# Performance work log

Measured on AMD Instinct MI355X. Metric: run time of the kernel, lower is better.

The kernel has to match this reference:

```python
import jax, jax.numpy as jnp
import numpy as np

D = 256
H = 256
B = 128
T = 512


def _init_cell(key, input_size, hidden_size):
    K = 1.0 / np.sqrt(hidden_size)
    k1, k2, k3, k4 = jax.random.split(key, 4)
    u = lambda k, shape: jax.random.uniform(k, shape, jnp.float32, -K, K)
    return (u(k1, (3 * hidden_size, input_size)),
            u(k2, (3 * hidden_size, hidden_size)),
            u(k3, (3 * hidden_size,)),
            u(k4, (3 * hidden_size,)))


def setup_inputs() -> dict:
    key = jax.random.key(0)
    kx, kf, kb = jax.random.split(key, 3)
    x = jax.random.normal(kx, (B, T, D), dtype=jnp.float32)
    w_ih_fw, w_hh_fw, b_ih_fw, b_hh_fw = _init_cell(kf, D, H)
    w_ih_bw, w_hh_bw, b_ih_bw, b_hh_bw = _init_cell(kb, D, H)
    return {
        "x": x,
        "w_ih_fw": w_ih_fw, "w_hh_fw": w_hh_fw, "b_ih_fw": b_ih_fw, "b_hh_fw": b_hh_fw,
        "w_ih_bw": w_ih_bw, "w_hh_bw": w_hh_bw, "b_ih_bw": b_ih_bw, "b_hh_bw": b_hh_bw,
    }


def _gru_scan(x_tbd, w_ih, w_hh, b_ih, b_hh):
    # x_tbd: [T, B, D]; returns outputs [T, B, H] and final h [B, H]
    h0 = jnp.zeros((x_tbd.shape[1], H), dtype=x_tbd.dtype)

    def step(h, x_t):
        xT = x_t @ w_ih.T + b_ih          # [B, 3H]
        hT = h @ w_hh.T + b_hh            # [B, 3H]
        s = jax.nn.sigmoid(xT + hT)
        r = s[:, :H]
        z = s[:, H:2 * H]
        n = jnp.tanh(xT[:, 2 * H:] + r * hT[:, 2 * H:])
        h_new = (1.0 - z) * n + z * h
        return h_new, h_new

    h_last, outs = jax.lax.scan(step, h0, x_tbd)
    return outs, h_last


def reference(x, w_ih_fw, w_hh_fw, b_ih_fw, b_hh_fw,
              w_ih_bw, w_hh_bw, b_ih_bw, b_hh_bw):
    x_tbd = jnp.swapaxes(x, 0, 1)                         # [T, B, D]
    outs_fw, h_fw = _gru_scan(x_tbd, w_ih_fw, w_hh_fw, b_ih_fw, b_hh_fw)
    outs_bw_rev, h_bw = _gru_scan(x_tbd[::-1], w_ih_bw, w_hh_bw, b_ih_bw, b_hh_bw)
    outs_bw = outs_bw_rev[::-1]
    outputs = jnp.concatenate([outs_fw, outs_bw], axis=-1)  # [T, B, 2H]
    outputs = jnp.swapaxes(outputs, 0, 1)                   # [B, T, 2H]
    return outputs, h_fw, h_bw
```

## Files before the change

### kernel.cpp

```cpp
#include <hip/hip_runtime.h>
#include <stdint.h>
#include <stddef.h>

#define T_ 512
#define B_ 128
#define D_ 256
#define H_ 256
#define NR 768
#define ROWS 65536
#define OUT_MAIN 33554432ull

typedef __attribute__((ext_vector_type(4))) float f32x4;
typedef __attribute__((ext_vector_type(8))) short s16x8;

__device__ __forceinline__ unsigned short f2bf(float f) {
    union { float f; uint32_t u; } v; v.f = f;
    return (unsigned short)((v.u + 0x7FFFu + ((v.u >> 16) & 1u)) >> 16);
}
__device__ __forceinline__ float bf2f(unsigned short h) {
    union { uint32_t u; float f; } v; v.u = ((uint32_t)h) << 16;
    return v.f;
}
__device__ __forceinline__ float sigm(float x) { return 1.f / (1.f + __expf(-x)); }
__device__ __forceinline__ float tanh_(float x) {
    float e = __expf(2.f * x);
    return 1.f - 2.f / (e + 1.f);
}
__device__ __forceinline__ s16x8 pack8(const float* f) {
    union { s16x8 v; unsigned short u[8]; } p;
#pragma unroll
    for (int i = 0; i < 8; ++i) p.u[i] = f2bf(f[i]);
    return p.v;
}

__global__ void k_convert(const float* __restrict__ wf, const float* __restrict__ wb,
                          unsigned short* __restrict__ dst) {
    int i = blockIdx.x * blockDim.x + threadIdx.x;
    const int n = NR * D_;
    if (i < n) dst[i] = f2bf(wf[i]);
    else if (i < 2 * n) dst[i] = f2bf(wb[i - n]);
}

__global__ __launch_bounds__(512, 2) void k_xgemm(
    const float* __restrict__ x, const unsigned short* __restrict__ wbf,
    const float* __restrict__ bih_f, const float* __restrict__ bhh_f,
    const float* __restrict__ bih_b, const float* __restrict__ bhh_b,
    unsigned short* __restrict__ XT)
{
    __shared__ __align__(16) unsigned short lds_a[128 * 72];
    const int tid = threadIdx.x;
    const int lane = tid & 63, wid = tid >> 6;
    const int wm = wid >> 2, wn = wid & 3;
    const int t = blockIdx.x;
    const int cblk = blockIdx.y * 384;

    f32x4 acc[4][6];
#pragma unroll
    for (int m = 0; m < 4; ++m)
#pragma unroll
        for (int n = 0; n < 6; ++n) acc[m][n] = (f32x4){0.f, 0.f, 0.f, 0.f};

    for (int kb = 0; kb < 4; ++kb) {
        if (kb) __syncthreads();
        {
            int row = tid >> 2, seg = tid & 3;
            const float* src = x + ((size_t)row * T_ + t) * D_ + kb * 64 + seg * 16;
            float fv[16];
            *(f32x4*)&fv[0]  = *(const f32x4*)(src);
            *(f32x4*)&fv[4]  = *(const f32x4*)(src + 4);
            *(f32x4*)&fv[8]  = *(const f32x4*)(src + 8);
            *(f32x4*)&fv[12] = *(const f32x4*)(src + 12);
            *(s16x8*)&lds_a[row * 72 + seg * 16]     = pack8(&fv[0]);
            *(s16x8*)&lds_a[row * 72 + seg * 16 + 8] = pack8(&fv[8]);
        }
        __syncthreads();
#pragma unroll
        for (int kt = 0; kt < 2; ++kt) {
            s16x8 av[4];
#pragma unroll
            for (int mt = 0; mt < 4; ++mt) {
                int r = wm * 64 + mt * 16 + (lane & 15);
                av[mt] = *(const s16x8*)&lds_a[r * 72 + kt * 32 + (lane >> 4) * 8];
            }
#pragma unroll
            for (int nt = 0; nt < 6; ++nt) {
                int c = cblk + wn * 96 + nt * 16 + (lane & 15);
                const unsigned short* bs = wbf + (size_t)c * D_ + kb * 64 + kt * 32 + (lane >> 4) * 8;
                s16x8 bv = *(const s16x8*)bs;
#pragma unroll
                for (int mt = 0; mt < 4; ++mt)
                    acc[mt][nt] = __builtin_amdgcn_mfma_f32_16x16x32_bf16(av[mt], bv, acc[mt][nt], 0, 0, 0);
            }
        }
    }
    const int dir = (cblk >= NR) ? 1 : 0;
    const float* bih = dir ? bih_b : bih_f;
    const float* bhh = dir ? bhh_b : bhh_f;
#pragma unroll
    for (int nt = 0; nt < 6; ++nt) {
        int c = cblk + wn * 96 + nt * 16 + (lane & 15);
        int cc = c - dir * NR;
        float bias = bih[cc] + (cc < 512 ? bhh[cc] : 0.f);
#pragma unroll
        for (int mt = 0; mt < 4; ++mt) {
#pragma unroll
            for (int q = 0; q < 4; ++q) {
                int rr = wm * 64 + mt * 16 + (lane >> 4) * 4 + q;
                size_t off = ((size_t)dir * ROWS + (size_t)t * B_ + rr) * NR + cc;
                XT[off] = f2bf(acc[mt][nt][q] + bias);
            }
        }
    }
}

__global__ __launch_bounds__(512, 2) void k_recur(
    const float* __restrict__ whh_f, const float* __restrict__ whh_b,
    const float* __restrict__ bhh_f, const float* __restrict__ bhh_b,
    const unsigned short* __restrict__ XT,
    float* __restrict__ out)
{
    __shared__ __align__(16) unsigned short xbuf[2][16 * 768];
    __shared__ __align__(16) unsigned short hlds[16 * 264];
    const int tid = threadIdx.x, lane = tid & 63, wid = tid >> 6;
    const int bid = blockIdx.x;
    const int dir = bid >> 3, b0 = (bid & 7) * 16;
    const float* whh = dir ? whh_b : whh_f;
    const float* bhh = dir ? bhh_b : bhh_f;

    s16x8 fB[6][8];
#pragma unroll
    for (int g = 0; g < 3; ++g) {
#pragma unroll
        for (int half = 0; half < 2; ++half) {
            int nt = 2 * g + half;
            int cb = g * 256 + 32 * wid + half * 16;
#pragma unroll
            for (int k0 = 0; k0 < 8; ++k0) {
                const float* s = whh + (size_t)(cb + (lane & 15)) * H_ + k0 * 32 + (lane >> 4) * 8;
                float fv[8];
                *(f32x4*)&fv[0] = *(const f32x4*)(s);
                *(f32x4*)&fv[4] = *(const f32x4*)(s + 4);
                fB[nt][k0] = pack8(fv);
            }
        }
    }
    const float bhn0 = bhh[512 + 32 * wid + (lane & 15)];
    const float bhn1 = bhh[512 + 32 * wid + 16 + (lane & 15)];

    for (int i = tid; i < 16 * 264; i += 512) hlds[i] = 0;
    __syncthreads();

    const size_t xt_dir = (size_t)dir * ROWS;
    {
        int t0 = dir ? (T_ - 1) : 0;
        const char* g = (const char*)(XT + (xt_dir + (size_t)t0 * B_ + b0) * NR);
#pragma unroll
        for (int i = 0; i < 3; ++i)
            __builtin_amdgcn_global_load_lds(
                (const __attribute__((address_space(1))) uint32_t*)(g + i * 8192 + tid * 16),
                (__attribute__((address_space(3))) uint32_t*)((char*)&xbuf[0][0] + i * 8192 + wid * 1024),
                16, 0, 0);
    }

#pragma unroll 1
    for (int s = 0; s < T_; ++s) {
        const int t = dir ? (T_ - 1 - s) : s;
        const int t_next = dir ? (t > 0 ? t - 1 : 0) : (t < T_ - 1 ? t + 1 : t);
        {
            const char* g = (const char*)(XT + (xt_dir + (size_t)t_next * B_ + b0) * NR);
            char* l = (char*)&xbuf[(s + 1) & 1][0];
#pragma unroll
            for (int i = 0; i < 3; ++i)
                __builtin_amdgcn_global_load_lds(
                    (const __attribute__((address_space(1))) uint32_t*)(g + i * 8192 + tid * 16),
                    (__attribute__((address_space(3))) uint32_t*)(l + i * 8192 + wid * 1024),
                    16, 0, 0);
        }
        f32x4 acc[6];
#pragma unroll
        for (int n = 0; n < 6; ++n) acc[n] = (f32x4){0.f, 0.f, 0.f, 0.f};
#pragma unroll
        for (int k0 = 0; k0 < 8; ++k0) {
            s16x8 a = *(const s16x8*)&hlds[(lane & 15) * 264 + k0 * 32 + (lane >> 4) * 8];
#pragma unroll
            for (int nt = 0; nt < 6; ++nt)
                acc[nt] = __builtin_amdgcn_mfma_f32_16x16x32_bf16(a, fB[nt][k0], acc[nt], 0, 0, 0);
        }
        if (s == 0) asm volatile("s_waitcnt vmcnt(3) lgkmcnt(0)\n\ts_barrier" ::: "memory");
        else        asm volatile("s_waitcnt vmcnt(11) lgkmcnt(0)\n\ts_barrier" ::: "memory");

        const unsigned short* xb = &xbuf[s & 1][0];
#pragma unroll
        for (int jt = 0; jt < 2; ++jt) {
            const int j = 32 * wid + jt * 16 + (lane & 15);
            const float bn = jt ? bhn1 : bhn0;
#pragma unroll
            for (int q = 0; q < 4; ++q) {
                const int row = (lane >> 4) * 4 + q;
                float xr = bf2f(xb[row * 768 + j]);
                float xz = bf2f(xb[row * 768 + 256 + j]);
                float xn = bf2f(xb[row * 768 + 512 + j]);
                float hv = bf2f(hlds[row * 264 + j]);
                float rg = sigm(acc[jt][q] + xr);
                float zg = sigm(acc[2 + jt][q] + xz);
                float ng = tanh_(xn + rg * (acc[4 + jt][q] + bn));
                float hnew = ng + zg * (hv - ng);
                hlds[row * 264 + j] = f2bf(hnew);
                out[((size_t)(b0 + row) * T_ + t) * 512 + dir * 256 + j] = hnew;
                if (s == T_ - 1)
                    out[OUT_MAIN + (size_t)dir * B_ * H_ + (size_t)(b0 + row) * H_ + j] = hnew;
            }
        }
        asm volatile("s_waitcnt lgkmcnt(0)\n\ts_barrier" ::: "memory");
    }
}

extern "C" void kernel_launch(void* const* d_in, const int* in_sizes, int n_in,
                              void* d_out, int out_size, void* d_ws, size_t ws_size,
                              hipStream_t stream) {
    const float* x     = (const float*)d_in[0];
    const float* wih_f = (const float*)d_in[1];
    const float* whh_f = (const float*)d_in[2];
    const float* bih_f = (const float*)d_in[3];
    const float* bhh_f = (const float*)d_in[4];
    const float* wih_b = (const float*)d_in[5];
    const float* whh_b = (const float*)d_in[6];
    const float* bih_b = (const float*)d_in[7];
    const float* bhh_b = (const float*)d_in[8];
    float* out = (float*)d_out;

    unsigned short* wbf = (unsigned short*)d_ws;
    unsigned short* XT  = (unsigned short*)((char*)d_ws + 786432);

    k_convert<<<dim3(768), dim3(512), 0, stream>>>(wih_f, wih_b, wbf);
    k_xgemm<<<dim3(512, 4), dim3(512), 0, stream>>>(x, wbf, bih_f, bhh_f, bih_b, bhh_b, XT);
    k_recur<<<dim3(16), dim3(512), 0, stream>>>(whh_f, whh_b, bhh_f, bhh_b, XT, out);
}
```

Baseline: 1.751 ms.

## Prelayout input projections per thread and double-buffer hidden state in recurrence

The input-projection GEMM now writes its bf16 output in a per-(direction, batch group) layout where each recurrence thread's 24 needed values are contiguous, so the recurrent kernel loads them straight into registers with three 16-byte loads instead of staging them in LDS with global_load_lds. The hidden state is double-buffered in LDS (padded stride 280) and the step loop is unrolled by two, which removes one barrier per timestep. Sigmoid and tanh now use the hardware reciprocal approximation, and the GEMM grid is re-split by direction and batch half. The risks are register pressure from holding the prefetched projections and the slight precision loss from the approximate reciprocal.

```diff
diff --git a/kernel.cpp b/kernel.cpp
--- a/kernel.cpp
+++ b/kernel.cpp
@@ -7,8 +7,9 @@
 #define D_ 256
 #define H_ 256
 #define NR 768
-#define ROWS 65536
 #define OUT_MAIN 33554432ull
+#define XT_STRIDE 12288
+#define HB 280
 
 typedef __attribute__((ext_vector_type(4))) float f32x4;
 typedef __attribute__((ext_vector_type(8))) short s16x8;
@@ -21,10 +22,12 @@
     union { uint32_t u; float f; } v; v.u = ((uint32_t)h) << 16;
     return v.f;
 }
-__device__ __forceinline__ float sigm(float x) { return 1.f / (1.f + __expf(-x)); }
+__device__ __forceinline__ float sigm(float x) {
+    return __builtin_amdgcn_rcpf(1.f + __expf(-x));
+}
 __device__ __forceinline__ float tanh_(float x) {
     float e = __expf(2.f * x);
-    return 1.f - 2.f / (e + 1.f);
+    return 1.f - 2.f * __builtin_amdgcn_rcpf(e + 1.f);
 }
 __device__ __forceinline__ s16x8 pack8(const float* f) {
     union { s16x8 v; unsigned short u[8]; } p;
@@ -47,12 +50,11 @@
     const float* __restrict__ bih_b, const float* __restrict__ bhh_b,
     unsigned short* __restrict__ XT)
 {
-    __shared__ __align__(16) unsigned short lds_a[128 * 72];
+    __shared__ __align__(16) unsigned short lds_a[64 * 72];
     const int tid = threadIdx.x;
-    const int lane = tid & 63, wid = tid >> 6;
-    const int wm = wid >> 2, wn = wid & 3;
+    const int lane = tid & 63, wn = tid >> 6;
     const int t = blockIdx.x;
-    const int cblk = blockIdx.y * 384;
+    const int dir = blockIdx.y >> 1, mh = blockIdx.y & 1;
 
     f32x4 acc[4][6];
 #pragma unroll
@@ -63,15 +65,12 @@
     for (int kb = 0; kb < 4; ++kb) {
         if (kb) __syncthreads();
         {
-            int row = tid >> 2, seg = tid & 3;
-            const float* src = x + ((size_t)row * T_ + t) * D_ + kb * 64 + seg * 16;
-            float fv[16];
-            *(f32x4*)&fv[0]  = *(const f32x4*)(src);
-            *(f32x4*)&fv[4]  = *(const f32x4*)(src + 4);
-            *(f32x4*)&fv[8]  = *(const f32x4*)(src + 8);
-            *(f32x4*)&fv[12] = *(const f32x4*)(src + 12);
-            *(s16x8*)&lds_a[row * 72 + seg * 16]     = pack8(&fv[0]);
-            *(s16x8*)&lds_a[row * 72 + seg * 16 + 8] = pack8(&fv[8]);
+            int row = tid >> 3, seg = tid & 7;
+            const float* src = x + ((size_t)(mh * 64 + row) * T_ + t) * D_ + kb * 64 + seg * 8;
+            float fv[8];
+            *(f32x4*)&fv[0] = *(const f32x4*)(src);
+            *(f32x4*)&fv[4] = *(const f32x4*)(src + 4);
+            *(s16x8*)&lds_a[row * 72 + seg * 8] = pack8(fv);
         }
         __syncthreads();
 #pragma unroll
@@ -79,38 +78,96 @@
             s16x8 av[4];
 #pragma unroll
             for (int mt = 0; mt < 4; ++mt) {
-                int r = wm * 64 + mt * 16 + (lane & 15);
+                int r = mt * 16 + (lane & 15);
                 av[mt] = *(const s16x8*)&lds_a[r * 72 + kt * 32 + (lane >> 4) * 8];
             }
 #pragma unroll
             for (int nt = 0; nt < 6; ++nt) {
-                int c = cblk + wn * 96 + nt * 16 + (lane & 15);
-                const unsigned short* bs = wbf + (size_t)c * D_ + kb * 64 + kt * 32 + (lane >> 4) * 8;
-                s16x8 bv = *(const s16x8*)bs;
+                int c = dir * NR + wn * 96 + nt * 16 + (lane & 15);
+                s16x8 bv = *(const s16x8*)(wbf + (size_t)c * D_ + kb * 64 + kt * 32 + (lane >> 4) * 8);
 #pragma unroll
                 for (int mt = 0; mt < 4; ++mt)
                     acc[mt][nt] = __builtin_amdgcn_mfma_f32_16x16x32_bf16(av[mt], bv, acc[mt][nt], 0, 0, 0);
             }
         }
     }
-    const int dir = (cblk >= NR) ? 1 : 0;
     const float* bih = dir ? bih_b : bih_f;
     const float* bhh = dir ? bhh_b : bhh_f;
 #pragma unroll
     for (int nt = 0; nt < 6; ++nt) {
-        int c = cblk + wn * 96 + nt * 16 + (lane & 15);
-        int cc = c - dir * NR;
-        float bias = bih[cc] + (cc < 512 ? bhh[cc] : 0.f);
+        const int cw = wn * 96 + nt * 16 + (lane & 15);
+        const int gate = cw >> 8, j = cw & 255;
+        const int jt = (j >> 4) & 1;
+        const int rtid = (j >> 5) * 64 + (((lane >> 4)) << 4) + (j & 15);
+        float bias = bih[cw] + (cw < 512 ? bhh[cw] : 0.f);
 #pragma unroll
         for (int mt = 0; mt < 4; ++mt) {
 #pragma unroll
             for (int q = 0; q < 4; ++q) {
-                int rr = wm * 64 + mt * 16 + (lane >> 4) * 4 + q;
-                size_t off = ((size_t)dir * ROWS + (size_t)t * B_ + rr) * NR + cc;
-                XT[off] = f2bf(acc[mt][nt][q] + bias);
-            }
-        }
-    }
+                int rr = mh * 64 + mt * 16 + (lane >> 4) * 4 + q;
+                int bgrp = rr >> 4;
+                int v = (jt * 4 + q) * 3 + gate;
+                XT[((size_t)(dir * 8 + bgrp) * T_ + t) * XT_STRIDE + (size_t)rtid * 24 + v]
+                    = f2bf(acc[mt][nt][q] + bias);
+            }
+        }
+    }
+}
+
+template<int P>
+__device__ __forceinline__ void gru_step(
+    int s, int dir, int b0, int tid, int lane, int wid,
+    const unsigned short* __restrict__ XTw, float* __restrict__ out,
+    unsigned short* hb, const s16x8 (&fB)[6][8], float bhn0, float bhn1,
+    s16x8 (&CUR)[3], s16x8 (&NXT)[3])
+{
+    const int t  = dir ? (T_ - 1 - s) : s;
+    const int sn = (s < T_ - 1) ? s + 1 : s;
+    const int tn = dir ? (T_ - 1 - sn) : sn;
+    {
+        const s16x8* p = (const s16x8*)(XTw + (size_t)tn * XT_STRIDE) + (size_t)tid * 3;
+        NXT[0] = p[0]; NXT[1] = p[1]; NXT[2] = p[2];
+    }
+    const unsigned short* hr = hb + P * (16 * HB);
+    unsigned short*       hw = hb + (P ^ 1) * (16 * HB);
+
+    f32x4 acc[6];
+#pragma unroll
+    for (int n = 0; n < 6; ++n) acc[n] = (f32x4){0.f, 0.f, 0.f, 0.f};
+#pragma unroll
+    for (int k0 = 0; k0 < 8; ++k0) {
+        s16x8 a = *(const s16x8*)&hr[(lane & 15) * HB + k0 * 32 + (lane >> 4) * 8];
+#pragma unroll
+        for (int nt = 0; nt < 6; ++nt)
+            acc[nt] = __builtin_amdgcn_mfma_f32_16x16x32_bf16(a, fB[nt][k0], acc[nt], 0, 0, 0);
+    }
+#pragma unroll
+    for (int jt = 0; jt < 2; ++jt) {
+        const int j = 32 * wid + jt * 16 + (lane & 15);
+        const float bn = jt ? bhn1 : bhn0;
+#pragma unroll
+        for (int q = 0; q < 4; ++q) {
+            const int row = (lane >> 4) * 4 + q;
+            const int v = (jt * 4 + q) * 3;
+            float xr = bf2f((unsigned short)CUR[(v + 0) >> 3][(v + 0) & 7]);
+            float xz = bf2f((unsigned short)CUR[(v + 1) >> 3][(v + 1) & 7]);
+            float xn = bf2f((unsigned short)CUR[(v + 2) >> 3][(v + 2) & 7]);
+            float hv = bf2f(hr[row * HB + j]);
+            float rg = sigm(acc[jt][q] + xr);
+            float zg = sigm(acc[2 + jt][q] + xz);
+            float ng = tanh_(xn + rg * (acc[4 + jt][q] + bn));
+            float hnew = ng + zg * (hv - ng);
+            hw[row * HB + j] = f2bf(hnew);
+            size_t off = ((size_t)(b0 + row) << 18) + ((size_t)t << 9) + (size_t)dir * 256 + j;
+            out[off] = hnew;
+            if (s == T_ - 1)
+                out[OUT_MAIN + (size_t)dir * B_ * H_ + (size_t)(b0 + row) * H_ + j] = hnew;
+        }
+    }
+    __builtin_amdgcn_sched_barrier(0);
+    asm volatile("s_waitcnt lgkmcnt(0)");
+    __builtin_amdgcn_s_barrier();
+    __builtin_amdgcn_sched_barrier(0);
 }
 
 __global__ __launch_bounds__(512, 2) void k_recur(
@@ -119,8 +176,7 @@
     const unsigned short* __restrict__ XT,
     float* __restrict__ out)
 {
-    __shared__ __align__(16) unsigned short xbuf[2][16 * 768];
-    __shared__ __align__(16) unsigned short hlds[16 * 264];
+    __shared__ __align__(16) unsigned short hb[2 * 16 * HB];
     const int tid = threadIdx.x, lane = tid & 63, wid = tid >> 6;
     const int bid = blockIdx.x;
     const int dir = bid >> 3, b0 = (bid & 7) * 16;
@@ -136,10 +192,10 @@
             int cb = g * 256 + 32 * wid + half * 16;
 #pragma unroll
             for (int k0 = 0; k0 < 8; ++k0) {
-                const float* s = whh + (size_t)(cb + (lane & 15)) * H_ + k0 * 32 + (lane >> 4) * 8;
+                const float* sp = whh + (size_t)(cb + (lane & 15)) * H_ + k0 * 32 + (lane >> 4) * 8;
                 float fv[8];
-                *(f32x4*)&fv[0] = *(const f32x4*)(s);
-                *(f32x4*)&fv[4] = *(const f32x4*)(s + 4);
+                *(f32x4*)&fv[0] = *(const f32x4*)(sp);
+                *(f32x4*)&fv[4] = *(const f32x4*)(sp + 4);
                 fB[nt][k0] = pack8(fv);
             }
         }
@@ -147,71 +203,20 @@
     const float bhn0 = bhh[512 + 32 * wid + (lane & 15)];
     const float bhn1 = bhh[512 + 32 * wid + 16 + (lane & 15)];
 
-    for (int i = tid; i < 16 * 264; i += 512) hlds[i] = 0;
+    for (int i = tid; i < 16 * HB / 2; i += 512) ((uint32_t*)hb)[i] = 0;
     __syncthreads();
 
-    const size_t xt_dir = (size_t)dir * ROWS;
+    const unsigned short* XTw = XT + (size_t)(dir * 8 + (bid & 7)) * T_ * XT_STRIDE;
+    s16x8 XA[3], XB[3];
     {
-        int t0 = dir ? (T_ - 1) : 0;
-        const char* g = (const char*)(XT + (xt_dir + (size_t)t0 * B_ + b0) * NR);
-#pragma unroll
-        for (int i = 0; i < 3; ++i)
-            __builtin_amdgcn_global_load_lds(
-                (const __attribute__((address_space(1))) uint32_t*)(g + i * 8192 + tid * 16),
-                (__attribute__((address_space(3))) uint32_t*)((char*)&xbuf[0][0] + i * 8192 + wid * 1024),
-                16, 0, 0);
-    }
-
+        const int t0 = dir ? (T_ - 1) : 0;
+        const s16x8* p = (const s16x8*)(XTw + (size_t)t0 * XT_STRIDE) + (size_t)tid * 3;
+        XA[0] = p[0]; XA[1] = p[1]; XA[2] = p[2];
+    }
 #pragma unroll 1
-    for (int s = 0; s < T_; ++s) {
-        const int t = dir ? (T_ - 1 - s) : s;
-        const int t_next = dir ? (t > 0 ? t - 1 : 0) : (t < T_ - 1 ? t + 1 : t);
-        {
-            const char* g = (const char*)(XT + (xt_dir + (size_t)t_next * B_ + b0) * NR);
-            char* l = (char*)&xbuf[(s + 1) & 1][0];
-#pragma unroll
-            for (int i = 0; i < 3; ++i)
-                __builtin_amdgcn_global_load_lds(
-                    (const __attribute__((address_space(1))) uint32_t*)(g + i * 8192 + tid * 16),
-                    (__attribute__((address_space(3))) uint32_t*)(l + i * 8192 + wid * 1024),
-                    16, 0, 0);
-        }
-        f32x4 acc[6];
-#pragma unroll
-        for (int n = 0; n < 6; ++n) acc[n] = (f32x4){0.f, 0.f, 0.f, 0.f};
-#pragma unroll
-        for (int k0 = 0; k0 < 8; ++k0) {
-            s16x8 a = *(const s16x8*)&hlds[(lane & 15) * 264 + k0 * 32 + (lane >> 4) * 8];
-#pragma unroll
-            for (int nt = 0; nt < 6; ++nt)
-                acc[nt] = __builtin_amdgcn_mfma_f32_16x16x32_bf16(a, fB[nt][k0], acc[nt], 0, 0, 0);
-        }
-        if (s == 0) asm volatile("s_waitcnt vmcnt(3) lgkmcnt(0)\n\ts_barrier" ::: "memory");
-        else        asm volatile("s_waitcnt vmcnt(11) lgkmcnt(0)\n\ts_barrier" ::: "memory");
-
-        const unsigned short* xb = &xbuf[s & 1][0];
-#pragma unroll
-        for (int jt = 0; jt < 2; ++jt) {
-            const int j = 32 * wid + jt * 16 + (lane & 15);
-            const float bn = jt ? bhn1 : bhn0;
-#pragma unroll
-            for (int q = 0; q < 4; ++q) {
-                const int row = (lane >> 4) * 4 + q;
-                float xr = bf2f(xb[row * 768 + j]);
-                float xz = bf2f(xb[row * 768 + 256 + j]);
-                float xn = bf2f(xb[row * 768 + 512 + j]);
-                float hv = bf2f(hlds[row * 264 + j]);
-                float rg = sigm(acc[jt][q] + xr);
-                float zg = sigm(acc[2 + jt][q] + xz);
-                float ng = tanh_(xn + rg * (acc[4 + jt][q] + bn));
-                float hnew = ng + zg * (hv - ng);
-                hlds[row * 264 + j] = f2bf(hnew);
-                out[((size_t)(b0 + row) * T_ + t) * 512 + dir * 256 + j] = hnew;
-                if (s == T_ - 1)
-                    out[OUT_MAIN + (size_t)dir * B_ * H_ + (size_t)(b0 + row) * H_ + j] = hnew;
-            }
-        }
-        asm volatile("s_waitcnt lgkmcnt(0)\n\ts_barrier" ::: "memory");
+    for (int s = 0; s < T_; s += 2) {
+        gru_step<0>(s,     dir, b0, tid, lane, wid, XTw, out, hb, fB, bhn0, bhn1, XA, XB);
+        gru_step<1>(s + 1, dir, b0, tid, lane, wid, XTw, out, hb, fB, bhn0, bhn1, XB, XA);
     }
 }
 
```

Result: faster. 1.695 ms (-3.2%).
